# Optimization experiments

Measured on AMD Instinct MI355X. Metric: run time of the kernel, lower is better.

Reference implementation:

```python
import jax, jax.numpy as jnp
import numpy as np

NQ = 8          # n_qubits (attention and ffn)
DIM = 2 ** NQ   # state-vector dimension
EPS = 1e-5      # nn.LayerNorm default eps


def _layernorm(x, g, b):
    m = jnp.mean(x, axis=-1, keepdims=True)
    v = jnp.mean((x - m) ** 2, axis=-1, keepdims=True)
    return (x - m) * jax.lax.rsqrt(v + EPS) * g + b


def _attn_quantum(tok, theta):
    """Batched 8-qubit state-vector sim: RX(tok_i)+RX(theta_i) per wire, CNOT ring, <Z_i>.
    tok: [N, 8] -> returns [N, 8]."""
    N = tok.shape[0]
    half = 0.5 * (tok + theta)  # RX(a)RX(b) = RX(a+b) on same wire
    # per-wire amplitude RX(a)|0> = (cos(a/2), -i sin(a/2))
    re = jnp.stack([jnp.cos(half), jnp.zeros_like(half)], axis=-1)
    im = jnp.stack([jnp.zeros_like(half), -jnp.sin(half)], axis=-1)
    amp = jax.lax.complex(re, im)  # [N, 8, 2]
    # build product state with wire 0 as the leading qubit axis: [N, 2, ..., 2]
    state = amp[:, 0, :]
    for w in range(1, NQ):
        state = state[..., None] * amp[:, w, :].reshape((N,) + (1,) * w + (2,))
    # CNOT ring: (0,1),(1,2),...,(6,7),(7,0)
    pairs = [(i, i + 1) for i in range(NQ - 1)] + [(NQ - 1, 0)]
    for c, t in pairs:
        flipped = jnp.flip(state, axis=t + 1)
        mask = jnp.arange(2).reshape((1,) * (c + 1) + (2,) + (1,) * (NQ - 1 - c))
        state = jnp.where(mask == 1, flipped, state)
    probs = (state.real ** 2 + state.imag ** 2).reshape(N, DIM)
    # <Z_w> = sum_k probs[k] * (1 - 2*bit_w(k)); wire 0 is most significant bit
    bits = (jnp.arange(DIM)[None, :] >> (NQ - 1 - jnp.arange(NQ)[:, None])) & 1
    signs = (1.0 - 2.0 * bits).astype(probs.dtype)  # [8, 256]
    return probs @ signs.T


def _ffn_quantum(tok, phi):
    """Product state per wire: RY(phi_i) RX(tok_i) |0>, then <Z_i>. tok: [..., 8]."""
    ct, st = jnp.cos(0.5 * tok), jnp.sin(0.5 * tok)
    cp, sp = jnp.cos(0.5 * phi), jnp.sin(0.5 * phi)
    # v0 = cp*ct + i*sp*st ; v1 = sp*ct - i*cp*st ; z = |v0|^2 - |v1|^2
    return (cp * ct) ** 2 + (sp * st) ** 2 - (sp * ct) ** 2 - (cp * st) ** 2


def setup_inputs() -> dict:
    key = jax.random.key(0)
    ks = jax.random.split(key, 8)
    B, S, E, F = 32, 2048, 8, 2048
    x = jax.random.normal(ks[0], (B, S, E), dtype=jnp.float32)
    theta = jax.random.uniform(ks[1], (NQ,), dtype=jnp.float32, minval=-np.pi, maxval=np.pi)
    phi = jax.random.uniform(ks[2], (NQ,), dtype=jnp.float32, minval=-np.pi, maxval=np.pi)
    W1 = jax.random.normal(ks[3], (F, NQ), dtype=jnp.float32) / np.sqrt(NQ)
    b1 = jax.random.normal(ks[4], (F,), dtype=jnp.float32) * 0.01
    W2 = jax.random.normal(ks[5], (E, F), dtype=jnp.float32) / np.sqrt(F)
    b2 = jax.random.normal(ks[6], (E,), dtype=jnp.float32) * 0.01
    gamma1 = jnp.ones((E,), dtype=jnp.float32)
    beta1 = jnp.zeros((E,), dtype=jnp.float32)
    gamma2 = jnp.ones((E,), dtype=jnp.float32)
    beta2 = jnp.zeros((E,), dtype=jnp.float32)
    return {"x": x, "theta": theta, "phi": phi, "W1": W1, "b1": b1, "W2": W2,
            "b2": b2, "gamma1": gamma1, "beta1": beta1, "gamma2": gamma2, "beta2": beta2}


def reference(x, theta, phi, W1, b1, W2, b2, gamma1, beta1, gamma2, beta2):
    B, S, E = x.shape
    attn = _attn_quantum(x.reshape(B * S, E), theta).reshape(B, S, E)
    h = _layernorm(x + attn, gamma1, beta1)            # dropout is identity (eval)
    z = _ffn_quantum(h, phi)                            # [B, S, 8]
    f = jax.nn.relu(z @ W1.T + b1) @ W2.T + b2          # linear1 -> relu -> linear2
    return _layernorm(h + f, gamma2, beta2)
```

## Files before the change

### kernel.cpp

```cpp
#include <hip/hip_runtime.h>
#include <math.h>

#define NQ 8
#define FDIM 2048
#define EPSV 1e-5f

typedef __attribute__((ext_vector_type(8))) short short8v;
typedef __attribute__((ext_vector_type(16))) float f32x16;

__device__ __forceinline__ unsigned pk_bf16(float lo, float hi) {
    unsigned r;
    asm("v_cvt_pk_bf16_f32 %0, %1, %2" : "=v"(r) : "v"(lo), "v"(hi));
    return r;
}

__device__ __forceinline__ short8v pack4(unsigned a, unsigned b, unsigned c, unsigned d) {
    uint4 w; w.x = a; w.y = b; w.z = c; w.w = d;
    return __builtin_bit_cast(short8v, w);
}

__launch_bounds__(768, 3)
__global__ void qtb_kernel(const float* __restrict__ x,
                           const float* __restrict__ theta,
                           const float* __restrict__ phi,
                           const float* __restrict__ W1,
                           const float* __restrict__ b1,
                           const float* __restrict__ W2,
                           const float* __restrict__ b2,
                           const float* __restrict__ g1,
                           const float* __restrict__ be1,
                           const float* __restrict__ g2,
                           const float* __restrict__ be2,
                           float* __restrict__ out)
{
    __shared__ short W1f[64 * 512];
    __shared__ short W2s[8 * 2056];
    __shared__ float park[12][512];
    __shared__ float hLds[256 * 8];

    const int tid = threadIdx.x;

    for (int k = tid; k < FDIM; k += 768) {
        const float4 wa = *reinterpret_cast<const float4*>(W1 + (size_t)k * NQ);
        const float4 wb = *reinterpret_cast<const float4*>(W1 + (size_t)k * NQ + 4);
        const float bk = b1[k];
        unsigned* d0 = reinterpret_cast<unsigned*>(&W1f[(k >> 5) * 512 + (k & 31) * 8]);
        unsigned* d1 = reinterpret_cast<unsigned*>(&W1f[(k >> 5) * 512 + ((k & 31) + 32) * 8]);
        d0[0] = pk_bf16(wa.x, wa.y); d0[1] = pk_bf16(wa.z, wa.w);
        d0[2] = pk_bf16(bk, 0.f);    d0[3] = 0u;
        d1[0] = pk_bf16(wb.x, wb.y); d1[1] = pk_bf16(wb.z, wb.w);
        d1[2] = 0u;                  d1[3] = 0u;
    }
    for (int idx = tid; idx < 8 * 1024; idx += 768) {
        const int i = idx >> 10, kp = idx & 1023;
        const int k0 = kp * 2;
        const float2 w = *reinterpret_cast<const float2*>(W2 + (size_t)i * FDIM + k0);
        const int quad = (k0 >> 2) & 3;
        const int posq = (0x3120 >> (quad * 4)) & 0xF;
        const int dcol = (k0 & ~15) | (posq * 4 + (k0 & 3));
        *reinterpret_cast<unsigned*>(&W2s[i * 2056 + dcol]) = pk_bf16(w.x, w.y);
    }
    __syncthreads();

    const int lane = tid & 63;
    const int wid  = tid >> 6;
    const int q    = wid >> 2;
    const int g    = wid & 3;
    const int hi2  = lane >> 5;
    const int il   = lane & 31;
    const int token = blockIdx.x * 256 + g * 64 + lane;

    const float4 xa = reinterpret_cast<const float4*>(x + (size_t)token * NQ)[0];
    const float4 xb = reinterpret_cast<const float4*>(x + (size_t)token * NQ)[1];
    float xv[8] = {xa.x, xa.y, xa.z, xa.w, xb.x, xb.y, xb.z, xb.w};

    float c[8];
#pragma unroll
    for (int j = 0; j < 8; ++j) c[j] = __cosf(xv[j] + theta[j]);
    float attn[8];
    attn[0] = ((c[1] * c[2]) * (c[3] * c[4])) * ((c[5] * c[6]) * c[7]);
    {
        float p = c[0];
#pragma unroll
        for (int j = 1; j < 8; ++j) { p *= c[j]; attn[j] = p; }
    }
    float s[8];
#pragma unroll
    for (int j = 0; j < 8; ++j) s[j] = xv[j] + attn[j];
    float mean = 0.f;
#pragma unroll
    for (int j = 0; j < 8; ++j) mean += s[j];
    mean *= 0.125f;
    float var = 0.f;
#pragma unroll
    for (int j = 0; j < 8; ++j) { float d = s[j] - mean; var = fmaf(d, d, var); }
    var *= 0.125f;
    const float rs = rsqrtf(var + EPSV);
    float h[8];
#pragma unroll
    for (int j = 0; j < 8; ++j) h[j] = (s[j] - mean) * rs * g1[j] + be1[j];

    float zv[8];
#pragma unroll
    for (int j = 0; j < 8; ++j) zv[j] = __cosf(phi[j]) * __cosf(h[j]);

    if (q == 0) {
        float4* hp = reinterpret_cast<float4*>(&hLds[(g * 64 + lane) * 8]);
        hp[0] = make_float4(h[0], h[1], h[2], h[3]);
        hp[1] = make_float4(h[4], h[5], h[6], h[7]);
    }

    unsigned zpk[4];
#pragma unroll
    for (int p = 0; p < 4; ++p) zpk[p] = pk_bf16(zv[2 * p], zv[2 * p + 1]);
    unsigned zApk[4], zBpk[4];
#pragma unroll
    for (int p = 0; p < 4; ++p) {
        zApk[p] = (unsigned)__shfl((int)zpk[p], il);
        zBpk[p] = (unsigned)__shfl((int)zpk[p], 32 + il);
    }
    const unsigned biasv = 0x00003f80u;
    const short8v b1A = pack4(hi2 ? zApk[2] : zApk[0],
                              hi2 ? zApk[3] : zApk[1],
                              hi2 ? 0u : biasv, 0u);
    const short8v b1B = pack4(hi2 ? zBpk[2] : zBpk[0],
                              hi2 ? zBpk[3] : zBpk[1],
                              hi2 ? 0u : biasv, 0u);

    f32x16 zeroC;
#pragma unroll
    for (int e = 0; e < 16; ++e) zeroC[e] = 0.f;
    f32x16 accA = zeroC, accB = zeroC;

    const int ir = il & 7;

    const int lo = q * 21;
    const int hi = (q == 2) ? 64 : lo + 21;

#pragma unroll 2
    for (int cc = lo; cc < hi; ++cc) {
        const short8v A1 = *reinterpret_cast<const short8v*>(&W1f[cc * 512 + lane * 8]);
        const short* w2base = &W2s[ir * 2056 + cc * 32];
        const short8v B0 = *reinterpret_cast<const short8v*>(w2base + hi2 * 8);
        const short8v B1 = *reinterpret_cast<const short8v*>(w2base + 16 + hi2 * 8);

        f32x16 C1A = __builtin_amdgcn_mfma_f32_32x32x16_bf16(A1, b1A, zeroC, 0, 0, 0);
        const short8v a0A = pack4(
            pk_bf16(fmaxf(C1A[0], 0.f), fmaxf(C1A[1], 0.f)),
            pk_bf16(fmaxf(C1A[2], 0.f), fmaxf(C1A[3], 0.f)),
            pk_bf16(fmaxf(C1A[4], 0.f), fmaxf(C1A[5], 0.f)),
            pk_bf16(fmaxf(C1A[6], 0.f), fmaxf(C1A[7], 0.f)));
        const short8v a1A = pack4(
            pk_bf16(fmaxf(C1A[8], 0.f),  fmaxf(C1A[9], 0.f)),
            pk_bf16(fmaxf(C1A[10], 0.f), fmaxf(C1A[11], 0.f)),
            pk_bf16(fmaxf(C1A[12], 0.f), fmaxf(C1A[13], 0.f)),
            pk_bf16(fmaxf(C1A[14], 0.f), fmaxf(C1A[15], 0.f)));

        f32x16 C1B = __builtin_amdgcn_mfma_f32_32x32x16_bf16(A1, b1B, zeroC, 0, 0, 0);
        const short8v a0B = pack4(
            pk_bf16(fmaxf(C1B[0], 0.f), fmaxf(C1B[1], 0.f)),
            pk_bf16(fmaxf(C1B[2], 0.f), fmaxf(C1B[3], 0.f)),
            pk_bf16(fmaxf(C1B[4], 0.f), fmaxf(C1B[5], 0.f)),
            pk_bf16(fmaxf(C1B[6], 0.f), fmaxf(C1B[7], 0.f)));
        const short8v a1B = pack4(
            pk_bf16(fmaxf(C1B[8], 0.f),  fmaxf(C1B[9], 0.f)),
            pk_bf16(fmaxf(C1B[10], 0.f), fmaxf(C1B[11], 0.f)),
            pk_bf16(fmaxf(C1B[12], 0.f), fmaxf(C1B[13], 0.f)),
            pk_bf16(fmaxf(C1B[14], 0.f), fmaxf(C1B[15], 0.f)));

        accA = __builtin_amdgcn_mfma_f32_32x32x16_bf16(a0A, B0, accA, 0, 0, 0);
        accA = __builtin_amdgcn_mfma_f32_32x32x16_bf16(a1A, B1, accA, 0, 0, 0);
        accB = __builtin_amdgcn_mfma_f32_32x32x16_bf16(a0B, B0, accB, 0, 0, 0);
        accB = __builtin_amdgcn_mfma_f32_32x32x16_bf16(a1B, B1, accB, 0, 0, 0);
    }

    if (il < 8) {
        float* fb = &park[wid][0];
#pragma unroll
        for (int r = 0; r < 16; ++r) {
            const int trow = (r & 3) + 8 * (r >> 2) + 4 * hi2;
            fb[trow * 8 + il]        = accA[r];
            fb[(32 + trow) * 8 + il] = accB[r];
        }
    }
    __syncthreads();

    if (q == 0) {
        float fv[8] = {0.f, 0.f, 0.f, 0.f, 0.f, 0.f, 0.f, 0.f};
#pragma unroll
        for (int qq = 0; qq < 3; ++qq) {
            const float* pb = &park[qq * 4 + g][lane * 8];
            const float4 f0 = *reinterpret_cast<const float4*>(pb);
            const float4 f1 = *reinterpret_cast<const float4*>(pb + 4);
            fv[0] += f0.x; fv[1] += f0.y; fv[2] += f0.z; fv[3] += f0.w;
            fv[4] += f1.x; fv[5] += f1.y; fv[6] += f1.z; fv[7] += f1.w;
        }

        const float4 h0 = reinterpret_cast<const float4*>(&hLds[(g * 64 + lane) * 8])[0];
        const float4 h1 = reinterpret_cast<const float4*>(&hLds[(g * 64 + lane) * 8])[1];
        const float hv[8] = {h0.x, h0.y, h0.z, h0.w, h1.x, h1.y, h1.z, h1.w};

        float y[8];
#pragma unroll
        for (int j = 0; j < 8; ++j) y[j] = hv[j] + fv[j] + b2[j];
        float mean2 = 0.f;
#pragma unroll
        for (int j = 0; j < 8; ++j) mean2 += y[j];
        mean2 *= 0.125f;
        float var2 = 0.f;
#pragma unroll
        for (int j = 0; j < 8; ++j) { float d = y[j] - mean2; var2 = fmaf(d, d, var2); }
        var2 *= 0.125f;
        const float rs2 = rsqrtf(var2 + EPSV);

        float o[8];
#pragma unroll
        for (int j = 0; j < 8; ++j) o[j] = (y[j] - mean2) * rs2 * g2[j] + be2[j];

        float4* op = reinterpret_cast<float4*>(out + (size_t)token * NQ);
        op[0] = make_float4(o[0], o[1], o[2], o[3]);
        op[1] = make_float4(o[4], o[5], o[6], o[7]);
    }
}

extern "C" void kernel_launch(void* const* d_in, const int* in_sizes, int n_in,
                              void* d_out, int out_size, void* d_ws, size_t ws_size,
                              hipStream_t stream) {
    const float* x     = (const float*)d_in[0];
    const float* theta = (const float*)d_in[1];
    const float* phi   = (const float*)d_in[2];
    const float* W1    = (const float*)d_in[3];
    const float* b1    = (const float*)d_in[4];
    const float* W2    = (const float*)d_in[5];
    const float* b2    = (const float*)d_in[6];
    const float* g1    = (const float*)d_in[7];
    const float* be1   = (const float*)d_in[8];
    const float* g2    = (const float*)d_in[9];
    const float* be2   = (const float*)d_in[10];
    float* out = (float*)d_out;

    const int ntok = in_sizes[0] / NQ;
    const int grid = ntok / 256;

    qtb_kernel<<<grid, 768, 0, stream>>>(x, theta, phi, W1, b1, W2, b2,
                                         g1, be1, g2, be2, out);
}
```

Baseline: 23.57 us.

## Software-pipeline FFN MFMA loop with double-buffered LDS operands

Restructures the inner FFN loop so that the first-layer MFMA for the next chunk is issued before the ReLU/pack and second-layer MFMAs of the current chunk. The W1 and W2 fragments for two chunks ahead are loaded from LDS into alternating registers. The aim is to hide MFMA result latency and LDS load latency behind independent work. In exchange it raises register pressure, which matters under the 768-thread, 3-block launch bounds, and adds wraparound index logic for the prefetches.

```diff
diff --git a/kernel.cpp b/kernel.cpp
--- a/kernel.cpp
+++ b/kernel.cpp
@@ -18,6 +18,39 @@
     uint4 w; w.x = a; w.y = b; w.z = c; w.w = d;
     return __builtin_bit_cast(short8v, w);
 }
+
+#define ITER(AUSE, ALOAD, B0USE, B1USE, C2IDX)                                      \
+  {                                                                                 \
+    const short8v a0A = pack4(                                                      \
+        pk_bf16(fmaxf(C1A[0], 0.f),  fmaxf(C1A[1], 0.f)),                           \
+        pk_bf16(fmaxf(C1A[2], 0.f),  fmaxf(C1A[3], 0.f)),                           \
+        pk_bf16(fmaxf(C1A[4], 0.f),  fmaxf(C1A[5], 0.f)),                           \
+        pk_bf16(fmaxf(C1A[6], 0.f),  fmaxf(C1A[7], 0.f)));                          \
+    const short8v a1A = pack4(                                                      \
+        pk_bf16(fmaxf(C1A[8], 0.f),  fmaxf(C1A[9], 0.f)),                           \
+        pk_bf16(fmaxf(C1A[10], 0.f), fmaxf(C1A[11], 0.f)),                          \
+        pk_bf16(fmaxf(C1A[12], 0.f), fmaxf(C1A[13], 0.f)),                          \
+        pk_bf16(fmaxf(C1A[14], 0.f), fmaxf(C1A[15], 0.f)));                         \
+    C1A = __builtin_amdgcn_mfma_f32_32x32x16_bf16(AUSE, b1A, zeroC, 0, 0, 0);       \
+    const short8v a0B = pack4(                                                      \
+        pk_bf16(fmaxf(C1B[0], 0.f),  fmaxf(C1B[1], 0.f)),                           \
+        pk_bf16(fmaxf(C1B[2], 0.f),  fmaxf(C1B[3], 0.f)),                           \
+        pk_bf16(fmaxf(C1B[4], 0.f),  fmaxf(C1B[5], 0.f)),                           \
+        pk_bf16(fmaxf(C1B[6], 0.f),  fmaxf(C1B[7], 0.f)));                          \
+    const short8v a1B = pack4(                                                      \
+        pk_bf16(fmaxf(C1B[8], 0.f),  fmaxf(C1B[9], 0.f)),                           \
+        pk_bf16(fmaxf(C1B[10], 0.f), fmaxf(C1B[11], 0.f)),                          \
+        pk_bf16(fmaxf(C1B[12], 0.f), fmaxf(C1B[13], 0.f)),                          \
+        pk_bf16(fmaxf(C1B[14], 0.f), fmaxf(C1B[15], 0.f)));                         \
+    C1B = __builtin_amdgcn_mfma_f32_32x32x16_bf16(AUSE, b1B, zeroC, 0, 0, 0);       \
+    accA = __builtin_amdgcn_mfma_f32_32x32x16_bf16(a0A, B0USE, accA, 0, 0, 0);      \
+    accA = __builtin_amdgcn_mfma_f32_32x32x16_bf16(a1A, B1USE, accA, 0, 0, 0);      \
+    accB = __builtin_amdgcn_mfma_f32_32x32x16_bf16(a0B, B0USE, accB, 0, 0, 0);      \
+    accB = __builtin_amdgcn_mfma_f32_32x32x16_bf16(a1B, B1USE, accB, 0, 0, 0);      \
+    ALOAD = *reinterpret_cast<const short8v*>(W1p + (C2IDX) * 512);                 \
+    B0USE = *reinterpret_cast<const short8v*>(W2p + (C2IDX) * 32);                  \
+    B1USE = *reinterpret_cast<const short8v*>(W2p + (C2IDX) * 32 + 16);             \
+  }
 
 __launch_bounds__(768, 3)
 __global__ void qtb_kernel(const float* __restrict__ x,
@@ -133,45 +166,32 @@
     f32x16 accA = zeroC, accB = zeroC;
 
     const int ir = il & 7;
-
+    const int n  = (q == 2) ? 22 : 21;
     const int lo = q * 21;
-    const int hi = (q == 2) ? 64 : lo + 21;
-
-#pragma unroll 2
-    for (int cc = lo; cc < hi; ++cc) {
-        const short8v A1 = *reinterpret_cast<const short8v*>(&W1f[cc * 512 + lane * 8]);
-        const short* w2base = &W2s[ir * 2056 + cc * 32];
-        const short8v B0 = *reinterpret_cast<const short8v*>(w2base + hi2 * 8);
-        const short8v B1 = *reinterpret_cast<const short8v*>(w2base + 16 + hi2 * 8);
-
-        f32x16 C1A = __builtin_amdgcn_mfma_f32_32x32x16_bf16(A1, b1A, zeroC, 0, 0, 0);
-        const short8v a0A = pack4(
-            pk_bf16(fmaxf(C1A[0], 0.f), fmaxf(C1A[1], 0.f)),
-            pk_bf16(fmaxf(C1A[2], 0.f), fmaxf(C1A[3], 0.f)),
-            pk_bf16(fmaxf(C1A[4], 0.f), fmaxf(C1A[5], 0.f)),
-            pk_bf16(fmaxf(C1A[6], 0.f), fmaxf(C1A[7], 0.f)));
-        const short8v a1A = pack4(
-            pk_bf16(fmaxf(C1A[8], 0.f),  fmaxf(C1A[9], 0.f)),
-            pk_bf16(fmaxf(C1A[10], 0.f), fmaxf(C1A[11], 0.f)),
-            pk_bf16(fmaxf(C1A[12], 0.f), fmaxf(C1A[13], 0.f)),
-            pk_bf16(fmaxf(C1A[14], 0.f), fmaxf(C1A[15], 0.f)));
-
-        f32x16 C1B = __builtin_amdgcn_mfma_f32_32x32x16_bf16(A1, b1B, zeroC, 0, 0, 0);
-        const short8v a0B = pack4(
-            pk_bf16(fmaxf(C1B[0], 0.f), fmaxf(C1B[1], 0.f)),
-            pk_bf16(fmaxf(C1B[2], 0.f), fmaxf(C1B[3], 0.f)),
-            pk_bf16(fmaxf(C1B[4], 0.f), fmaxf(C1B[5], 0.f)),
-            pk_bf16(fmaxf(C1B[6], 0.f), fmaxf(C1B[7], 0.f)));
-        const short8v a1B = pack4(
-            pk_bf16(fmaxf(C1B[8], 0.f),  fmaxf(C1B[9], 0.f)),
-            pk_bf16(fmaxf(C1B[10], 0.f), fmaxf(C1B[11], 0.f)),
-            pk_bf16(fmaxf(C1B[12], 0.f), fmaxf(C1B[13], 0.f)),
-            pk_bf16(fmaxf(C1B[14], 0.f), fmaxf(C1B[15], 0.f)));
-
-        accA = __builtin_amdgcn_mfma_f32_32x32x16_bf16(a0A, B0, accA, 0, 0, 0);
-        accA = __builtin_amdgcn_mfma_f32_32x32x16_bf16(a1A, B1, accA, 0, 0, 0);
-        accB = __builtin_amdgcn_mfma_f32_32x32x16_bf16(a0B, B0, accB, 0, 0, 0);
-        accB = __builtin_amdgcn_mfma_f32_32x32x16_bf16(a1B, B1, accB, 0, 0, 0);
+
+    const short* W1p = &W1f[lane * 8];
+    const short* W2p = &W2s[ir * 2056 + hi2 * 8];
+
+    short8v A1a = *reinterpret_cast<const short8v*>(W1p + lo * 512);
+    short8v B0a = *reinterpret_cast<const short8v*>(W2p + lo * 32);
+    short8v B1a = *reinterpret_cast<const short8v*>(W2p + lo * 32 + 16);
+    f32x16 C1A = __builtin_amdgcn_mfma_f32_32x32x16_bf16(A1a, b1A, zeroC, 0, 0, 0);
+    f32x16 C1B = __builtin_amdgcn_mfma_f32_32x32x16_bf16(A1a, b1B, zeroC, 0, 0, 0);
+    short8v A1b = *reinterpret_cast<const short8v*>(W1p + (lo + 1) * 512);
+    short8v B0b = *reinterpret_cast<const short8v*>(W2p + (lo + 1) * 32);
+    short8v B1b = *reinterpret_cast<const short8v*>(W2p + (lo + 1) * 32 + 16);
+
+    int t = 0;
+#pragma unroll 1
+    for (; t + 1 < n; t += 2) {
+        int c2 = t + 2; if (c2 >= n) c2 -= n; c2 += lo;
+        int c3 = t + 3; if (c3 >= n) c3 -= n; c3 += lo;
+        ITER(A1b, A1a, B0a, B1a, c2);
+        ITER(A1a, A1b, B0b, B1b, c3);
+    }
+    if (t < n) {
+        int c2 = t + 2 - n + lo;
+        ITER(A1b, A1a, B0a, B1a, c2);
     }
 
     if (il < 8) {
```

Result: faster. 22.60 us (-4.1%).
